# Optimization experiments

Hardware: AMD Instinct MI355X
Metric: run time of the kernel (lower is better)

The kernel has to match this reference:

```python
import jax, jax.numpy as jnp
import numpy as np

# Device/group constants for group_idx = 0 (from the source)
V_REF = 0.25
G_MIN = 1.0 / 983.3
G_MAX = 1.0 / 281.3
N_AVG = 2.132
N_STD = 0.095

P, N_IN, N_OUT = 1024, 784, 128


def setup_inputs() -> dict:
    key = jax.random.key(0)
    k1, k2, k3, k4, k5, k6 = jax.random.split(key, 6)
    x = jax.random.uniform(k1, (P, N_IN), dtype=jnp.float32)  # normalized pixel-like inputs in [0,1)
    stdv = 1.0 / np.sqrt(N_IN)
    w_pos = 0.5 + stdv * jax.random.normal(k2, (N_IN, N_OUT), dtype=jnp.float32)
    w_neg = 0.5 + stdv * jax.random.normal(k3, (N_IN, N_OUT), dtype=jnp.float32)
    b_pos = 0.5 * jnp.ones((N_OUT,), dtype=jnp.float32)
    b_neg = 0.5 * jnp.ones((N_OUT,), dtype=jnp.float32)
    # per-device nonlinearity parameter n ~ N(n_avg, n_std), crossbar shape (m, 2*n_out)
    n_param = N_AVG + N_STD * jax.random.normal(k4, (N_IN + 1, 2 * N_OUT), dtype=jnp.float32)
    return {"x": x, "w_pos": w_pos, "w_neg": w_neg, "b_pos": b_pos, "b_neg": b_neg, "n_param": n_param}


def reference(x, w_pos, w_neg, b_pos, b_neg, n_param):
    # --- build combined (weights+bias row), pos/neg column-interleaved crossbar params ---
    cw_pos = jnp.concatenate([w_pos, b_pos[None, :]], axis=0)  # (m, n_out), m = n_in+1
    cw_neg = jnp.concatenate([w_neg, b_neg[None, :]], axis=0)  # (m, n_out)
    m = cw_pos.shape[0]
    weights = jnp.stack([cw_pos, cw_neg], axis=-1).reshape(m, -1)  # (m, 2*n_out), interleaved

    max_weight = jnp.max(jnp.abs(weights))
    # w_params_to_G: linear map of nonnegative weight params onto [G_min, G_max]
    G = G_MIN + (G_MAX - G_MIN) * weights / max_weight  # (m, 2n)

    # x_to_V with appended ones column (bias word line)
    k_V = 2.0 * V_REF
    ones = jnp.ones((x.shape[0], 1), dtype=x.dtype)
    inputs = jnp.concatenate([x, ones], axis=1)  # (p, m)
    V = k_V * inputs  # (p, m)

    # nonlinear IV: I(V) = sign(V) * G*V_ref * n ** log2(|V|/V_ref)
    exponent = jnp.log2(jnp.maximum(jnp.abs(V), 1e-12) / V_REF)  # (p, m)
    I_ind = jnp.sign(V)[:, :, None] * (V_REF * G)[None, :, :] * n_param[None, :, :] ** exponent[:, :, None]  # (p, m, 2n)
    I = jnp.sum(I_ind, axis=1)  # bit-line currents, (p, 2n)

    # I_to_y: differential pos-neg columns, undo conductance/voltage scaling
    I_total = I[:, 0::2] - I[:, 1::2]  # (p, n_out)
    y = I_total * (max_weight / (k_V * (G_MAX - G_MIN)))
    return y
```

## Files before the change

kernel.cpp:

```cpp
#include <hip/hip_runtime.h>
#include <hip/hip_bf16.h>

#define P_ROWS   1024
#define N_IN     784
#define N_OUT    128
#define M_ROWS   785

#define RATIO_F  ((float)((1.0/983.3) / ((1.0/281.3) - (1.0/983.3))))
#define L_AVG_F  1.0922076f
#define LN2_F    0.6931472f

#define NCHK   11
#define MCH    72
#define NSTEP  9
#define NB_MAIN (64 * NCHK)

#define NB_MAX 64

typedef _Float16 half8 __attribute__((ext_vector_type(8)));
typedef float    f32x4 __attribute__((ext_vector_type(4)));

__global__ __launch_bounds__(256) void max_reduce_zero(
        const float* __restrict__ wp, const float* __restrict__ wn,
        const float* __restrict__ bp, const float* __restrict__ bn,
        float* __restrict__ partial, float4* __restrict__ out4) {
    const int b = blockIdx.x, t = threadIdx.x;

    const float4 z = make_float4(0.f, 0.f, 0.f, 0.f);
    #pragma unroll
    for (int i = 0; i < 2; ++i)
        out4[(size_t)b * 512 + i * 256 + t] = z;

    const int nW4 = (N_IN * N_OUT) / 4;
    const float4* wp4 = (const float4*)wp;
    const float4* wn4 = (const float4*)wn;
    int gid = b * 256 + t;
    float v = 0.0f;
    if (gid < N_OUT / 4) {
        float4 a = ((const float4*)bp)[gid], c = ((const float4*)bn)[gid];
        v = fmaxf(fmaxf(fmaxf(fabsf(a.x), fabsf(a.y)), fmaxf(fabsf(a.z), fabsf(a.w))),
                  fmaxf(fmaxf(fabsf(c.x), fabsf(c.y)), fmaxf(fabsf(c.z), fabsf(c.w))));
    }
    for (int i = gid; i < nW4; i += NB_MAX * 256) {
        float4 a = wp4[i], c = wn4[i];
        v = fmaxf(v, fmaxf(fmaxf(fabsf(a.x), fabsf(a.y)), fmaxf(fabsf(a.z), fabsf(a.w))));
        v = fmaxf(v, fmaxf(fmaxf(fabsf(c.x), fabsf(c.y)), fmaxf(fabsf(c.z), fabsf(c.w))));
    }
    for (int off = 32; off > 0; off >>= 1)
        v = fmaxf(v, __shfl_down(v, off, 64));
    __shared__ float smax[4];
    if ((t & 63) == 0) smax[t >> 6] = v;
    __syncthreads();
    if (t == 0)
        partial[b] = fmaxf(fmaxf(smax[0], smax[1]), fmaxf(smax[2], smax[3]));
}

__device__ __forceinline__ void genB(int m, int n, float c0,
        const float* __restrict__ wp, const float* __restrict__ wn,
        const float* __restrict__ npar, float C[4]) {
    float wpv = wp[(size_t)m * N_OUT + n];
    float wnv = wn[(size_t)m * N_OUT + n];
    float2 nv = *(const float2*)(npar + (size_t)m * (2 * N_OUT) + 2 * n);
    float Dp = LN2_F * (__builtin_amdgcn_logf(nv.x) - L_AVG_F);
    float Dn = LN2_F * (__builtin_amdgcn_logf(nv.y) - L_AVG_F);
    float Ap = c0 + 0.5f * wpv;
    float An = c0 + 0.5f * wnv;
    float ApD = Ap * Dp,    AnD = An * Dn;
    float ApD2 = ApD * Dp,  AnD2 = AnD * Dn;
    float ApD3 = ApD2 * Dp, AnD3 = AnD2 * Dn;
    C[0] = Ap - An;
    C[1] = ApD - AnD;
    C[2] = (ApD2 - AnD2) * 0.5f;
    C[3] = (ApD3 - AnD3) * (1.0f / 6.0f);
}

__device__ __forceinline__ void genBias(int n, float c0,
        const float* __restrict__ bp, const float* __restrict__ bn,
        const float* __restrict__ npar, float C[4]) {
    float wpv = bp[n];
    float wnv = bn[n];
    float2 nv = *(const float2*)(npar + (size_t)N_IN * (2 * N_OUT) + 2 * n);
    float Dp = LN2_F * (__builtin_amdgcn_logf(nv.x) - L_AVG_F);
    float Dn = LN2_F * (__builtin_amdgcn_logf(nv.y) - L_AVG_F);
    float Ap = c0 + 0.5f * wpv;
    float An = c0 + 0.5f * wnv;
    float ApD = Ap * Dp,    AnD = An * Dn;
    float ApD2 = ApD * Dp,  AnD2 = AnD * Dn;
    float ApD3 = ApD2 * Dp, AnD3 = AnD2 * Dn;
    C[0] = Ap - An;
    C[1] = ApD - AnD;
    C[2] = (ApD2 - AnD2) * 0.5f;
    C[3] = (ApD3 - AnD3) * (1.0f / 6.0f);
}

__global__ __launch_bounds__(256, 3) void memristor_main(
        const float* __restrict__ x,
        const float* __restrict__ wp, const float* __restrict__ wn,
        const float* __restrict__ bp, const float* __restrict__ bn,
        const float* __restrict__ npar, const float* __restrict__ partial,
        float* __restrict__ out) {
    const int bid = blockIdx.x;
    const int ch  = bid % NCHK;
    const int pb  = bid / NCHK;
    const int p0  = pb * 16;
    const int m0  = ch * MCH;
    const int t   = threadIdx.x;

    float mw = 0.0f;
    #pragma unroll
    for (int i = 0; i < NB_MAX; ++i) mw = fmaxf(mw, partial[i]);
    const float c0 = 0.5f * RATIO_F * mw;

    __shared__ half8 F_lds[36 * 16];
    const int NF4 = MCH / 4;
    for (int idx = t; idx < 16 * NF4; idx += 256) {
        const int p     = idx / NF4;
        const int f4    = idx - p * NF4;
        const int mbase = m0 + f4 * 4;
        float xv[4];
        if (mbase + 3 < N_IN) {
            float4 v = *(const float4*)(x + (size_t)(p0 + p) * N_IN + mbase);
            xv[0] = v.x; xv[1] = v.y; xv[2] = v.z; xv[3] = v.w;
        } else {
            #pragma unroll
            for (int u = 0; u < 4; ++u) {
                int m = mbase + u;
                xv[u] = (m < N_IN) ? x[(size_t)(p0 + p) * N_IN + m] : -1.0f;
            }
        }
        #pragma unroll
        for (int u = 0; u < 4; ++u) {
            const int m  = mbase + u;
            const int ml = m - m0;
            float e;
            if (m < N_IN)
                e = (xv[u] > 0.0f) ? __builtin_amdgcn_logf(2.0f * xv[u]) : -1.0e4f;
            else
                e = (m == N_IN) ? 1.0f : -1.0e4f;
            float F0 = __builtin_amdgcn_exp2f(e * L_AVG_F);
            float F1 = F0 * e, F2 = F1 * e, F3 = F2 * e;
            _Float16* dst = (_Float16*)&F_lds[(ml >> 1) * 16 + p] + (ml & 1) * 4;
            dst[0] = (_Float16)F0;
            dst[1] = (_Float16)F1;
            dst[2] = (_Float16)F2;
            dst[3] = (_Float16)F3;
        }
    }
    __syncthreads();

    const int lane = t & 63;
    const int w    = t >> 6;
    const int quad = lane >> 4;
    const int col  = lane & 15;
    const int n0   = w * 32;
    const int nA   = n0 + col;
    const int nB   = n0 + 16 + col;
    const int mq   = m0 + quad * 2;

    f32x4 acc0 = {0.f, 0.f, 0.f, 0.f};
    f32x4 acc1 = {0.f, 0.f, 0.f, 0.f};
    #pragma unroll
    for (int s = 0; s < NSTEP; ++s) {
        half8 a = F_lds[(s * 4 + quad) * 16 + col];
        half8 b0, b1;
        if (s < 8 || ch != NCHK - 1) {
            #pragma unroll
            for (int bb = 0; bb < 2; ++bb) {
                const int m = mq + s * 8 + bb;
                float CA[4], CB[4];
                genB(m, nA, c0, wp, wn, npar, CA);
                genB(m, nB, c0, wp, wn, npar, CB);
                #pragma unroll
                for (int j = 0; j < 4; ++j) {
                    b0[bb * 4 + j] = (_Float16)CA[j];
                    b1[bb * 4 + j] = (_Float16)CB[j];
                }
            }
        } else {
            #pragma unroll
            for (int j = 0; j < 8; ++j) { b0[j] = (_Float16)0.f; b1[j] = (_Float16)0.f; }
            if (quad == 0) {
                float CA[4], CB[4];
                genBias(nA, c0, bp, bn, npar, CA);
                genBias(nB, c0, bp, bn, npar, CB);
                #pragma unroll
                for (int j = 0; j < 4; ++j) {
                    b0[j] = (_Float16)CA[j];
                    b1[j] = (_Float16)CB[j];
                }
            }
        }
        acc0 = __builtin_amdgcn_mfma_f32_16x16x32_f16(a, b0, acc0, 0, 0, 0);
        acc1 = __builtin_amdgcn_mfma_f32_16x16x32_f16(a, b1, acc1, 0, 0, 0);
    }

    float* obase = out + (size_t)(p0 + quad * 4) * N_OUT;
    #pragma unroll
    for (int r = 0; r < 4; ++r) {
        unsafeAtomicAdd(&obase[(size_t)r * N_OUT + n0 + col],      acc0[r]);
        unsafeAtomicAdd(&obase[(size_t)r * N_OUT + n0 + 16 + col], acc1[r]);
    }
}

extern "C" void kernel_launch(void* const* d_in, const int* in_sizes, int n_in,
                              void* d_out, int out_size, void* d_ws, size_t ws_size,
                              hipStream_t stream) {
    const float* x  = (const float*)d_in[0];
    const float* wp = (const float*)d_in[1];
    const float* wn = (const float*)d_in[2];
    const float* bp = (const float*)d_in[3];
    const float* bn = (const float*)d_in[4];
    const float* np = (const float*)d_in[5];
    float* out = (float*)d_out;

    float* partial = (float*)d_ws;

    max_reduce_zero<<<NB_MAX, 256, 0, stream>>>(wp, wn, bp, bn, partial, (float4*)out);
    memristor_main<<<NB_MAIN, 256, 0, stream>>>(x, wp, wn, bp, bn, np, partial, out);
}
```

Baseline: 77.24 us.

## Fuse max-reduction and output zeroing into main kernel via cooperative grid sync

Merges the separate max-reduce/zero kernel into the main kernel. All 704 blocks zero the output and reduce the weight maximum, then a cooperative grid-wide sync separates that phase from the reduction over the per-block partials and the MFMA phase. The goal is to remove one kernel launch and its boundary, and to overlap the max reduction with building the input features in LDS. In exchange it adds a grid barrier, requires all blocks to be co-resident, and makes every block reread 704 partials.

```diff
diff --git a/kernel.cpp b/kernel.cpp
--- a/kernel.cpp
+++ b/kernel.cpp
@@ -1,5 +1,7 @@
 #include <hip/hip_runtime.h>
-#include <hip/hip_bf16.h>
+#include <hip/hip_cooperative_groups.h>
+
+namespace cg = cooperative_groups;
 
 #define P_ROWS   1024
 #define N_IN     784
@@ -15,45 +17,8 @@
 #define NSTEP  9
 #define NB_MAIN (64 * NCHK)
 
-#define NB_MAX 64
-
 typedef _Float16 half8 __attribute__((ext_vector_type(8)));
 typedef float    f32x4 __attribute__((ext_vector_type(4)));
-
-__global__ __launch_bounds__(256) void max_reduce_zero(
-        const float* __restrict__ wp, const float* __restrict__ wn,
-        const float* __restrict__ bp, const float* __restrict__ bn,
-        float* __restrict__ partial, float4* __restrict__ out4) {
-    const int b = blockIdx.x, t = threadIdx.x;
-
-    const float4 z = make_float4(0.f, 0.f, 0.f, 0.f);
-    #pragma unroll
-    for (int i = 0; i < 2; ++i)
-        out4[(size_t)b * 512 + i * 256 + t] = z;
-
-    const int nW4 = (N_IN * N_OUT) / 4;
-    const float4* wp4 = (const float4*)wp;
-    const float4* wn4 = (const float4*)wn;
-    int gid = b * 256 + t;
-    float v = 0.0f;
-    if (gid < N_OUT / 4) {
-        float4 a = ((const float4*)bp)[gid], c = ((const float4*)bn)[gid];
-        v = fmaxf(fmaxf(fmaxf(fabsf(a.x), fabsf(a.y)), fmaxf(fabsf(a.z), fabsf(a.w))),
-                  fmaxf(fmaxf(fabsf(c.x), fabsf(c.y)), fmaxf(fabsf(c.z), fabsf(c.w))));
-    }
-    for (int i = gid; i < nW4; i += NB_MAX * 256) {
-        float4 a = wp4[i], c = wn4[i];
-        v = fmaxf(v, fmaxf(fmaxf(fabsf(a.x), fabsf(a.y)), fmaxf(fabsf(a.z), fabsf(a.w))));
-        v = fmaxf(v, fmaxf(fmaxf(fabsf(c.x), fabsf(c.y)), fmaxf(fabsf(c.z), fabsf(c.w))));
-    }
-    for (int off = 32; off > 0; off >>= 1)
-        v = fmaxf(v, __shfl_down(v, off, 64));
-    __shared__ float smax[4];
-    if ((t & 63) == 0) smax[t >> 6] = v;
-    __syncthreads();
-    if (t == 0)
-        partial[b] = fmaxf(fmaxf(smax[0], smax[1]), fmaxf(smax[2], smax[3]));
-}
 
 __device__ __forceinline__ void genB(int m, int n, float c0,
         const float* __restrict__ wp, const float* __restrict__ wn,
@@ -93,11 +58,11 @@
     C[3] = (ApD3 - AnD3) * (1.0f / 6.0f);
 }
 
-__global__ __launch_bounds__(256, 3) void memristor_main(
+__global__ __launch_bounds__(256, 3) void memristor_fused(
         const float* __restrict__ x,
         const float* __restrict__ wp, const float* __restrict__ wn,
         const float* __restrict__ bp, const float* __restrict__ bn,
-        const float* __restrict__ npar, const float* __restrict__ partial,
+        const float* __restrict__ npar, float* __restrict__ partial,
         float* __restrict__ out) {
     const int bid = blockIdx.x;
     const int ch  = bid % NCHK;
@@ -106,10 +71,33 @@
     const int m0  = ch * MCH;
     const int t   = threadIdx.x;
 
-    float mw = 0.0f;
-    #pragma unroll
-    for (int i = 0; i < NB_MAX; ++i) mw = fmaxf(mw, partial[i]);
-    const float c0 = 0.5f * RATIO_F * mw;
+    {
+        float4* out4 = (float4*)out;
+        const float4 z = make_float4(0.f, 0.f, 0.f, 0.f);
+        for (int i = bid * 256 + t; i < (P_ROWS * N_OUT) / 4; i += NB_MAIN * 256)
+            out4[i] = z;
+    }
+
+    float v = 0.0f;
+    {
+        const int nW4 = (N_IN * N_OUT) / 4;
+        const float4* wp4 = (const float4*)wp;
+        const float4* wn4 = (const float4*)wn;
+        for (int i = bid * 256 + t; i < nW4; i += NB_MAIN * 256) {
+            float4 a = wp4[i], c = wn4[i];
+            v = fmaxf(v, fmaxf(fmaxf(fabsf(a.x), fabsf(a.y)), fmaxf(fabsf(a.z), fabsf(a.w))));
+            v = fmaxf(v, fmaxf(fmaxf(fabsf(c.x), fabsf(c.y)), fmaxf(fabsf(c.z), fabsf(c.w))));
+        }
+        if (bid == 0 && t < N_OUT / 4) {
+            float4 a = ((const float4*)bp)[t], c = ((const float4*)bn)[t];
+            v = fmaxf(v, fmaxf(fmaxf(fabsf(a.x), fabsf(a.y)), fmaxf(fabsf(a.z), fabsf(a.w))));
+            v = fmaxf(v, fmaxf(fmaxf(fabsf(c.x), fabsf(c.y)), fmaxf(fabsf(c.z), fabsf(c.w))));
+        }
+        for (int off = 32; off > 0; off >>= 1)
+            v = fmaxf(v, __shfl_down(v, off, 64));
+    }
+    __shared__ float smax[4];
+    if ((t & 63) == 0) smax[t >> 6] = v;
 
     __shared__ half8 F_lds[36 * 16];
     const int NF4 = MCH / 4;
@@ -119,8 +107,8 @@
         const int mbase = m0 + f4 * 4;
         float xv[4];
         if (mbase + 3 < N_IN) {
-            float4 v = *(const float4*)(x + (size_t)(p0 + p) * N_IN + mbase);
-            xv[0] = v.x; xv[1] = v.y; xv[2] = v.z; xv[3] = v.w;
+            float4 vx = *(const float4*)(x + (size_t)(p0 + p) * N_IN + mbase);
+            xv[0] = vx.x; xv[1] = vx.y; xv[2] = vx.z; xv[3] = vx.w;
         } else {
             #pragma unroll
             for (int u = 0; u < 4; ++u) {
@@ -147,6 +135,23 @@
         }
     }
     __syncthreads();
+    if (t == 0)
+        partial[bid] = fmaxf(fmaxf(smax[0], smax[1]), fmaxf(smax[2], smax[3]));
+
+    cg::this_grid().sync();
+
+    __shared__ float sred[4];
+    {
+        float pv = 0.0f;
+        for (int i = t; i < NB_MAIN; i += 256)
+            pv = fmaxf(pv, partial[i]);
+        for (int off = 32; off > 0; off >>= 1)
+            pv = fmaxf(pv, __shfl_down(pv, off, 64));
+        if ((t & 63) == 0) sred[t >> 6] = pv;
+    }
+    __syncthreads();
+    const float mw = fmaxf(fmaxf(sred[0], sred[1]), fmaxf(sred[2], sred[3]));
+    const float c0 = 0.5f * RATIO_F * mw;
 
     const int lane = t & 63;
     const int w    = t >> 6;
@@ -215,6 +220,8 @@
 
     float* partial = (float*)d_ws;
 
-    max_reduce_zero<<<NB_MAX, 256, 0, stream>>>(wp, wn, bp, bn, partial, (float4*)out);
-    memristor_main<<<NB_MAIN, 256, 0, stream>>>(x, wp, wn, bp, bn, np, partial, out);
-}
+    void* args[] = {(void*)&x, (void*)&wp, (void*)&wn, (void*)&bp,
+                    (void*)&bn, (void*)&np, (void*)&partial, (void*)&out};
+    hipLaunchCooperativeKernel((const void*)memristor_fused,
+                               dim3(NB_MAIN), dim3(256), args, 0, stream);
+}
```

Result: slower. 138.3 us (+79.1%).

## Retile main kernel to 32 rows by 64 outputs per block to halve B generation

Applied to the files above, without the earlier changes.

Each block now covers 32 input rows and half of the output columns (64) instead of 16 rows and all 128 columns. Each warp builds one B fragment per step and reuses it across two A fragments read from a larger LDS tile. Before, each warp built two B fragments sharing one A fragment. Per-block B generation work (loads of w_pos/w_neg/n_param plus logs) is halved, and total B generation across the grid also halves because more rows share each B tile. In exchange the block does twice the A-side exp/log preprocessing and uses twice the LDS.

```diff
diff --git a/kernel.cpp b/kernel.cpp
--- a/kernel.cpp
+++ b/kernel.cpp
@@ -13,7 +13,8 @@
 #define NCHK   11
 #define MCH    72
 #define NSTEP  9
-#define NB_MAIN (64 * NCHK)
+#define NPB    32
+#define NB_MAIN (NPB * 2 * NCHK)
 
 #define NB_MAX 64
 
@@ -101,8 +102,10 @@
         float* __restrict__ out) {
     const int bid = blockIdx.x;
     const int ch  = bid % NCHK;
-    const int pb  = bid / NCHK;
-    const int p0  = pb * 16;
+    const int rem = bid / NCHK;
+    const int pb  = rem >> 1;
+    const int nh  = rem & 1;
+    const int p0  = pb * 32;
     const int m0  = ch * MCH;
     const int t   = threadIdx.x;
 
@@ -111,9 +114,9 @@
     for (int i = 0; i < NB_MAX; ++i) mw = fmaxf(mw, partial[i]);
     const float c0 = 0.5f * RATIO_F * mw;
 
-    __shared__ half8 F_lds[36 * 16];
+    __shared__ half8 F_lds[36 * 32];
     const int NF4 = MCH / 4;
-    for (int idx = t; idx < 16 * NF4; idx += 256) {
+    for (int idx = t; idx < 32 * NF4; idx += 256) {
         const int p     = idx / NF4;
         const int f4    = idx - p * NF4;
         const int mbase = m0 + f4 * 4;
@@ -139,7 +142,7 @@
                 e = (m == N_IN) ? 1.0f : -1.0e4f;
             float F0 = __builtin_amdgcn_exp2f(e * L_AVG_F);
             float F1 = F0 * e, F2 = F1 * e, F3 = F2 * e;
-            _Float16* dst = (_Float16*)&F_lds[(ml >> 1) * 16 + p] + (ml & 1) * 4;
+            _Float16* dst = (_Float16*)&F_lds[(ml >> 1) * 32 + p] + (ml & 1) * 4;
             dst[0] = (_Float16)F0;
             dst[1] = (_Float16)F1;
             dst[2] = (_Float16)F2;
@@ -152,53 +155,47 @@
     const int w    = t >> 6;
     const int quad = lane >> 4;
     const int col  = lane & 15;
-    const int n0   = w * 32;
-    const int nA   = n0 + col;
-    const int nB   = n0 + 16 + col;
+    const int n    = nh * 64 + w * 16 + col;
     const int mq   = m0 + quad * 2;
 
     f32x4 acc0 = {0.f, 0.f, 0.f, 0.f};
     f32x4 acc1 = {0.f, 0.f, 0.f, 0.f};
     #pragma unroll
     for (int s = 0; s < NSTEP; ++s) {
-        half8 a = F_lds[(s * 4 + quad) * 16 + col];
-        half8 b0, b1;
+        half8 a0 = F_lds[(s * 4 + quad) * 32 + col];
+        half8 a1 = F_lds[(s * 4 + quad) * 32 + 16 + col];
+        half8 b;
         if (s < 8 || ch != NCHK - 1) {
             #pragma unroll
             for (int bb = 0; bb < 2; ++bb) {
                 const int m = mq + s * 8 + bb;
-                float CA[4], CB[4];
-                genB(m, nA, c0, wp, wn, npar, CA);
-                genB(m, nB, c0, wp, wn, npar, CB);
+                float C[4];
+                genB(m, n, c0, wp, wn, npar, C);
                 #pragma unroll
-                for (int j = 0; j < 4; ++j) {
-                    b0[bb * 4 + j] = (_Float16)CA[j];
-                    b1[bb * 4 + j] = (_Float16)CB[j];
-                }
+                for (int j = 0; j < 4; ++j)
+                    b[bb * 4 + j] = (_Float16)C[j];
             }
         } else {
             #pragma unroll
-            for (int j = 0; j < 8; ++j) { b0[j] = (_Float16)0.f; b1[j] = (_Float16)0.f; }
+            for (int j = 0; j < 8; ++j) b[j] = (_Float16)0.f;
             if (quad == 0) {
-                float CA[4], CB[4];
-                genBias(nA, c0, bp, bn, npar, CA);
-                genBias(nB, c0, bp, bn, npar, CB);
+                float C[4];
+                genBias(n, c0, bp, bn, npar, C);
                 #pragma unroll
-                for (int j = 0; j < 4; ++j) {
-                    b0[j] = (_Float16)CA[j];
-                    b1[j] = (_Float16)CB[j];
-                }
+                for (int j = 0; j < 4; ++j)
+                    b[j] = (_Float16)C[j];
             }
         }
-        acc0 = __builtin_amdgcn_mfma_f32_16x16x32_f16(a, b0, acc0, 0, 0, 0);
-        acc1 = __builtin_amdgcn_mfma_f32_16x16x32_f16(a, b1, acc1, 0, 0, 0);
-    }
-
-    float* obase = out + (size_t)(p0 + quad * 4) * N_OUT;
+        acc0 = __builtin_amdgcn_mfma_f32_16x16x32_f16(a0, b, acc0, 0, 0, 0);
+        acc1 = __builtin_amdgcn_mfma_f32_16x16x32_f16(a1, b, acc1, 0, 0, 0);
+    }
+
+    float* ob0 = out + (size_t)(p0 + quad * 4) * N_OUT + n;
+    float* ob1 = out + (size_t)(p0 + 16 + quad * 4) * N_OUT + n;
     #pragma unroll
     for (int r = 0; r < 4; ++r) {
-        unsafeAtomicAdd(&obase[(size_t)r * N_OUT + n0 + col],      acc0[r]);
-        unsafeAtomicAdd(&obase[(size_t)r * N_OUT + n0 + 16 + col], acc1[r]);
+        unsafeAtomicAdd(&ob0[(size_t)r * N_OUT], acc0[r]);
+        unsafeAtomicAdd(&ob1[(size_t)r * N_OUT], acc1[r]);
     }
 }
 
```

Measured after the change: 76.43 us. Within noise of the previous version (-1.0%).
